# Optimization experiments

Measured on AMD Instinct MI355X. Metric: run time of the kernel, lower is better.

## Reference

```python
import jax, jax.numpy as jnp
import numpy as np

N_NODES = 50000
N_EDGES = 800000
IN_DIM = 64
HID = 64
N_CLASSES = 10
NUM_GRAPHS = 512
EPS = 1e-5


def setup_inputs() -> dict:
    key = jax.random.key(0)
    ks = jax.random.split(key, 24)
    def w(k, shape, fan_in):
        return jax.random.normal(k, shape, jnp.float32) / np.sqrt(fan_in)
    inp = {
        "input_feature": jax.random.normal(ks[0], (N_NODES, IN_DIM), jnp.float32),
        "edge_src": jax.random.randint(ks[1], (N_EDGES,), 0, N_NODES, jnp.int32),
        "edge_dst": jax.random.randint(ks[2], (N_EDGES,), 0, N_NODES, jnp.int32),
        "graph_indicator": jnp.sort(jax.random.randint(ks[3], (N_NODES,), 0, NUM_GRAPHS, jnp.int32)),
        "labels": jax.random.randint(ks[4], (NUM_GRAPHS,), 0, N_CLASSES, jnp.int32),
        # GraphSAGE layer weights (self + neighbor paths) and biases
        "Ws1": w(ks[5], (IN_DIM, HID), IN_DIM), "Wn1": w(ks[6], (IN_DIM, HID), IN_DIM), "b1": jnp.zeros((HID,), jnp.float32),
        "Ws2": w(ks[7], (HID, HID), HID), "Wn2": w(ks[8], (HID, HID), HID), "b2": jnp.zeros((HID,), jnp.float32),
        "Ws3": w(ks[9], (HID, HID), HID), "Wn3": w(ks[10], (HID, HID), HID), "b3": jnp.zeros((HID,), jnp.float32),
        # BatchNorm affine params (bn1 output is discarded by the original forward, so omitted)
        "g2": jnp.ones((HID,), jnp.float32), "be2": jnp.zeros((HID,), jnp.float32),
        "g3": jnp.ones((HID,), jnp.float32), "be3": jnp.zeros((HID,), jnp.float32),
        # MLP head
        "fcW1": w(ks[11], (HID, 2 * HID), HID), "fcb1": jnp.zeros((2 * HID,), jnp.float32),
        "fcW2": w(ks[12], (2 * HID, HID), 2 * HID), "fcb2": jnp.zeros((HID,), jnp.float32),
        "fcW3": w(ks[13], (HID, N_CLASSES), HID), "fcb3": jnp.zeros((N_CLASSES,), jnp.float32),
    }
    return inp


def _batchnorm(x, g, b):
    # training-mode BN over the node dimension
    m = jnp.mean(x, axis=0)
    v = jnp.var(x, axis=0)
    return (x - m) * jax.lax.rsqrt(v + EPS) * g + b


def _sage(x, Ws, Wn, b, src, dst, inv_deg):
    # mean-aggregate neighbor features: agg[i] = mean_{(j->i) in E} x[j]
    msg = x[src]                                                   # [E, d] gather
    agg = jax.ops.segment_sum(msg, dst, num_segments=N_NODES)       # [N, d] scatter-add
    agg = agg * inv_deg                                             # mean aggregation
    return jax.nn.relu(x @ Ws + agg @ Wn + b)


def reference(input_feature, edge_src, edge_dst, graph_indicator, labels,
              Ws1, Wn1, b1, Ws2, Wn2, b2, Ws3, Wn3, b3,
              g2, be2, g3, be3, fcW1, fcb1, fcW2, fcb2, fcW3, fcb3):
    deg = jax.ops.segment_sum(jnp.ones((N_EDGES,), jnp.float32), edge_dst, num_segments=N_NODES)
    inv_deg = (1.0 / jnp.maximum(deg, 1.0))[:, None]                # [N, 1]
    # NOTE: original forward computes bn1(input_feature) but discards it (dead code)
    h = _sage(input_feature, Ws1, Wn1, b1, edge_src, edge_dst, inv_deg)
    h = _batchnorm(h, g2, be2)
    h = _sage(h, Ws2, Wn2, b2, edge_src, edge_dst, inv_deg)
    h = _batchnorm(h, g3, be3)
    h = _sage(h, Ws3, Wn3, b3, edge_src, edge_dst, inv_deg)
    # sum-pool per graph (labels only determine the number of graphs)
    pooled = jax.ops.segment_sum(h, graph_indicator, num_segments=NUM_GRAPHS)  # [G, HID]
    h = jax.nn.relu(pooled @ fcW1 + fcb1)
    h = jax.nn.relu(h @ fcW2 + fcb2)
    logits = h @ fcW3 + fcb3                                        # [G, num_classes]
    return logits
```

## Files before the change

### kernel.cpp

```cpp
#include <hip/hip_runtime.h>

#define N_NODES   50000
#define N_EDGES   800000
#define DIM       64
#define NUM_GRAPHS 512
#define EPS       1e-5f

#define SB   1024
#define NSB  ((N_NODES + SB - 1) / SB)

#define NBUCK ((N_NODES + 255) >> 8)
#define PA_E  4096
#define PA_B  ((N_EDGES + PA_E - 1) / PA_E)

__global__ void k_zero(int* __restrict__ deg, float* __restrict__ sums2,
                       float* __restrict__ sums3, float* __restrict__ pooled) {
    int i = blockIdx.x * 256 + threadIdx.x;
    if (i < N_NODES) deg[i] = 0;
    if (i < 128) { sums2[i] = 0.f; sums3[i] = 0.f; }
    if (i < NUM_GRAPHS * DIM) pooled[i] = 0.f;
}

__global__ void k_count(const int* __restrict__ dst, int* __restrict__ deg) {
    int i = blockIdx.x * 256 + threadIdx.x;
    if (i < N_EDGES) atomicAdd(&deg[dst[i]], 1);
}

__global__ void __launch_bounds__(1024)
k_scan1(const int* __restrict__ deg, int* __restrict__ bsum) {
    __shared__ int red[16];
    int t = threadIdx.x;
    int i = blockIdx.x * SB + t;
    int v = (i < N_NODES) ? deg[i] : 0;
#pragma unroll
    for (int d = 32; d; d >>= 1) v += __shfl_down(v, d, 64);
    if ((t & 63) == 0) red[t >> 6] = v;
    __syncthreads();
    if (t < 16) {
        int s = red[t];
#pragma unroll
        for (int d = 8; d; d >>= 1) s += __shfl_down(s, d, 16);
        if (t == 0) bsum[blockIdx.x] = s;
    }
}

__global__ void k_scan2(const int* __restrict__ bsum, int* __restrict__ boff) {
    int t = threadIdx.x;
    int v = (t < NSB) ? bsum[t] : 0;
    int orig = v;
#pragma unroll
    for (int d = 1; d < 64; d <<= 1) {
        int u = __shfl_up(v, d, 64);
        if (t >= d) v += u;
    }
    if (t < NSB) boff[t] = v - orig;
}

__global__ void __launch_bounds__(1024)
k_scan3(const int* __restrict__ deg, const int* __restrict__ boff,
        int* __restrict__ off, float* __restrict__ invd) {
    __shared__ int wsum[16];
    int t = threadIdx.x, lane = t & 63, w = t >> 6;
    int i = blockIdx.x * SB + t;
    int d = (i < N_NODES) ? deg[i] : 0;
    int v = d;
#pragma unroll
    for (int s = 1; s < 64; s <<= 1) {
        int u = __shfl_up(v, s, 64);
        if (lane >= s) v += u;
    }
    if (lane == 63) wsum[w] = v;
    __syncthreads();
    if (t < 16) {
        int x = wsum[t];
#pragma unroll
        for (int s = 1; s < 16; s <<= 1) {
            int u = __shfl_up(x, s, 16);
            if (t >= s) x += u;
        }
        wsum[t] = x;
    }
    __syncthreads();
    if (i < N_NODES) {
        int ex = boff[blockIdx.x] + ((w > 0) ? wsum[w - 1] : 0) + v - d;
        off[i] = ex;
        invd[i] = 1.0f / (float)max(d, 1);
        if (i == N_NODES - 1) off[N_NODES] = ex + d;
    }
}

__global__ void k_bcinit(const int* __restrict__ off, int* __restrict__ bcur) {
    int t = blockIdx.x * 256 + threadIdx.x;
    if (t < NBUCK) bcur[t] = off[t << 8];
}

__global__ void __launch_bounds__(1024)
k_passA(const int* __restrict__ src, const int* __restrict__ dst,
        int* __restrict__ bcur, unsigned long long* __restrict__ ebuf) {
    __shared__ int hist[NBUCK];
    __shared__ int gbase[NBUCK];
    int t = threadIdx.x;
    for (int i = t; i < NBUCK; i += 1024) hist[i] = 0;
    __syncthreads();
    int e0 = blockIdx.x * PA_E;
    int s0, s1, s2, s3, d0, d1, d2, d3, l0, l1, l2, l3;
    bool v0, v1, v2, v3;
    {
        int e = e0 + t;
        v0 = e < N_EDGES;
        s0 = v0 ? src[min(e, N_EDGES - 1)] : 0;
        d0 = v0 ? dst[min(e, N_EDGES - 1)] : 0;
        l0 = v0 ? atomicAdd(&hist[d0 >> 8], 1) : 0;
    }
    {
        int e = e0 + t + 1024;
        v1 = e < N_EDGES;
        s1 = v1 ? src[min(e, N_EDGES - 1)] : 0;
        d1 = v1 ? dst[min(e, N_EDGES - 1)] : 0;
        l1 = v1 ? atomicAdd(&hist[d1 >> 8], 1) : 0;
    }
    {
        int e = e0 + t + 2048;
        v2 = e < N_EDGES;
        s2 = v2 ? src[min(e, N_EDGES - 1)] : 0;
        d2 = v2 ? dst[min(e, N_EDGES - 1)] : 0;
        l2 = v2 ? atomicAdd(&hist[d2 >> 8], 1) : 0;
    }
    {
        int e = e0 + t + 3072;
        v3 = e < N_EDGES;
        s3 = v3 ? src[min(e, N_EDGES - 1)] : 0;
        d3 = v3 ? dst[min(e, N_EDGES - 1)] : 0;
        l3 = v3 ? atomicAdd(&hist[d3 >> 8], 1) : 0;
    }
    __syncthreads();
    if (t < NBUCK) {
        int h = hist[t];
        gbase[t] = h ? atomicAdd(&bcur[t], h) : 0;
    }
    __syncthreads();
    if (v0) ebuf[gbase[d0 >> 8] + l0] = ((unsigned long long)d0 << 32) | (unsigned)s0;
    if (v1) ebuf[gbase[d1 >> 8] + l1] = ((unsigned long long)d1 << 32) | (unsigned)s1;
    if (v2) ebuf[gbase[d2 >> 8] + l2] = ((unsigned long long)d2 << 32) | (unsigned)s2;
    if (v3) ebuf[gbase[d3 >> 8] + l3] = ((unsigned long long)d3 << 32) | (unsigned)s3;
}

__global__ void __launch_bounds__(1024)
k_passB(const unsigned long long* __restrict__ ebuf, const int* __restrict__ off,
        int* __restrict__ csr_src) {
    __shared__ int lcur[256];
    int base = blockIdx.x << 8;
    int nn = min(256, N_NODES - base);
    int t = threadIdx.x;
    if (t < nn) lcur[t] = off[base + t];
    __syncthreads();
    int js = off[base];
    int je = off[base + nn];
    for (int j = js + t; j < je; j += 1024) {
        unsigned long long pk = ebuf[j];
        int d = (int)(pk >> 32);
        int s = (int)(unsigned)pk;
        int pos = atomicAdd(&lcur[d - base], 1);
        csr_src[pos] = s;
    }
}

__device__ inline unsigned short f2bf(float f) {
    unsigned u = __float_as_uint(f);
    return (unsigned short)((u + 0x7FFFu + ((u >> 16) & 1u)) >> 16);
}

#define GR 32
template<bool BN>
__global__ void __launch_bounds__(256)
k_gemm(const float* __restrict__ x, const float* __restrict__ Ws,
       const float* __restrict__ Wn, const float* __restrict__ bias,
       const float* __restrict__ bn_a, const float* __restrict__ bn_c,
       float* __restrict__ xs, unsigned short* __restrict__ xnh16) {
    __shared__ float sX[GR][DIM];
    int tid = threadIdx.x;
    int lane = tid & 63, w = tid >> 6;

    float wsr[DIM], wnr[DIM];
#pragma unroll
    for (int k = 0; k < DIM; ++k) {
        wsr[k] = Ws[k * DIM + lane];
        wnr[k] = Wn[k * DIM + lane];
    }
    float bv = bias[lane];
    float aL = 1.f, cL = 0.f;
    if constexpr (BN) { aL = bn_a[lane]; cL = bn_c[lane]; }

    int rowBase = blockIdx.x * GR;
#pragma unroll
    for (int r = 0; r < GR / 4; ++r) {
        int row = r * 4 + w;
        int gr = rowBase + row;
        float v = (gr < N_NODES) ? x[gr * DIM + lane] : 0.f;
        sX[row][lane] = fmaf(v, aL, cL);
    }
    __syncthreads();

#pragma unroll
    for (int r = 0; r < 8; ++r) {
        int row = w * 8 + r;
        float s = bv, n = 0.f;
#pragma unroll
        for (int kg = 0; kg < DIM / 4; ++kg) {
            float4 xv = *reinterpret_cast<const float4*>(&sX[row][kg * 4]);
            s = fmaf(xv.x, wsr[kg * 4 + 0], s); n = fmaf(xv.x, wnr[kg * 4 + 0], n);
            s = fmaf(xv.y, wsr[kg * 4 + 1], s); n = fmaf(xv.y, wnr[kg * 4 + 1], n);
            s = fmaf(xv.z, wsr[kg * 4 + 2], s); n = fmaf(xv.z, wnr[kg * 4 + 2], n);
            s = fmaf(xv.w, wsr[kg * 4 + 3], s); n = fmaf(xv.w, wnr[kg * 4 + 3], n);
        }
        int grow = rowBase + row;
        if (grow < N_NODES) {
            xs[grow * DIM + lane] = s;
            xnh16[grow * DIM + lane] = f2bf(n);
        }
    }
}

template<bool POOL>
__global__ void __launch_bounds__(256)
k_agg(const float* __restrict__ xs, const unsigned* __restrict__ xnh,
      const int* __restrict__ off, const int* __restrict__ csr_src,
      const float* __restrict__ inv_deg, const int* __restrict__ gind,
      float* __restrict__ h, float* __restrict__ pooled) {
    int tid = threadIdx.x;
    int w = tid >> 6;
    int lane = tid & 63;
    int hw = lane >> 5;
    int p = lane & 31;
    int half_id = blockIdx.x * 8 + w * 2 + hw;
    int rA = half_id * 2;
    int rB = rA + 1;
    int jA = off[rA], jeA = off[rA + 1];
    int jB = jeA,     jeB = off[rB + 1];
    float axA = 0.f, ayA = 0.f, axB = 0.f, ayB = 0.f;

    while (jA < jeA || jB < jeB) {
#pragma unroll
        for (int k = 0; k < 4; ++k) {
            int iA = jA + k, iB = jB + k;
            bool vA = iA < jeA, vB = iB < jeB;
            int sA = csr_src[min(iA, N_EDGES - 1)];
            int sB = csr_src[min(iB, N_EDGES - 1)];
            sA = vA ? sA : 0;
            sB = vB ? sB : 0;
            unsigned wA = xnh[sA * 32 + p];
            unsigned wB = xnh[sB * 32 + p];
            axA += vA ? __uint_as_float(wA << 16) : 0.f;
            ayA += vA ? __uint_as_float(wA & 0xFFFF0000u) : 0.f;
            axB += vB ? __uint_as_float(wB << 16) : 0.f;
            ayB += vB ? __uint_as_float(wB & 0xFFFF0000u) : 0.f;
        }
        jA += 4; jB += 4;
    }

    float idA = inv_deg[rA], idB = inv_deg[rB];
    float2 xvA = *reinterpret_cast<const float2*>(&xs[rA * DIM + 2 * p]);
    float2 xvB = *reinterpret_cast<const float2*>(&xs[rB * DIM + 2 * p]);
    float vxA = fmaxf(fmaf(axA, idA, xvA.x), 0.f);
    float vyA = fmaxf(fmaf(ayA, idA, xvA.y), 0.f);
    float vxB = fmaxf(fmaf(axB, idB, xvB.x), 0.f);
    float vyB = fmaxf(fmaf(ayB, idB, xvB.y), 0.f);
    *reinterpret_cast<float2*>(&h[rA * DIM + 2 * p]) = make_float2(vxA, vyA);
    *reinterpret_cast<float2*>(&h[rB * DIM + 2 * p]) = make_float2(vxB, vyB);
    if constexpr (POOL) {
        int gA = gind[rA], gB = gind[rB];
        atomicAdd(&pooled[gA * DIM + 2 * p], vxA);
        atomicAdd(&pooled[gA * DIM + 2 * p + 1], vyA);
        atomicAdd(&pooled[gB * DIM + 2 * p], vxB);
        atomicAdd(&pooled[gB * DIM + 2 * p + 1], vyB);
    }
}

__global__ void __launch_bounds__(256)
k_stats(const float* __restrict__ h, float* __restrict__ sums) {
    int lane = threadIdx.x & 63, w = threadIdx.x >> 6;
    float s = 0.f, q = 0.f;
    for (int r = blockIdx.x * 4 + w; r < N_NODES; r += gridDim.x * 4) {
        float v = h[r * DIM + lane];
        s += v;
        q = fmaf(v, v, q);
    }
    __shared__ float sS[4][DIM], sQ[4][DIM];
    sS[w][lane] = s; sQ[w][lane] = q;
    __syncthreads();
    if (w == 0) {
        float ts = sS[0][lane] + sS[1][lane] + sS[2][lane] + sS[3][lane];
        float tq = sQ[0][lane] + sQ[1][lane] + sQ[2][lane] + sQ[3][lane];
        atomicAdd(&sums[lane], ts);
        atomicAdd(&sums[DIM + lane], tq);
    }
}

__global__ void k_bnfin(const float* __restrict__ sums, const float* __restrict__ g,
                        const float* __restrict__ be, float* __restrict__ a,
                        float* __restrict__ c) {
    int t = threadIdx.x;
    float m = sums[t] * (1.0f / N_NODES);
    float q = sums[DIM + t] * (1.0f / N_NODES);
    float v = q - m * m;
    float inv = 1.0f / sqrtf(v + EPS);
    float av = g[t] * inv;
    a[t] = av;
    c[t] = be[t] - m * av;
}

__global__ void __launch_bounds__(128)
k_mlp(const float* __restrict__ pooled,
      const float* __restrict__ W1, const float* __restrict__ b1,
      const float* __restrict__ W2, const float* __restrict__ b2,
      const float* __restrict__ W3, const float* __restrict__ b3,
      float* __restrict__ out) {
    __shared__ float sp[64], s1[128], s2[64];
    int g = blockIdx.x, t = threadIdx.x;
    if (t < 64) sp[t] = pooled[g * 64 + t];
    __syncthreads();
    {
        float acc = b1[t];
#pragma unroll
        for (int k = 0; k < 64; ++k) acc = fmaf(sp[k], W1[k * 128 + t], acc);
        s1[t] = fmaxf(acc, 0.f);
    }
    __syncthreads();
    if (t < 64) {
        float acc = b2[t];
#pragma unroll
        for (int k = 0; k < 128; ++k) acc = fmaf(s1[k], W2[k * 64 + t], acc);
        s2[t] = fmaxf(acc, 0.f);
    }
    __syncthreads();
    if (t < 10) {
        float acc = b3[t];
#pragma unroll
        for (int k = 0; k < 64; ++k) acc = fmaf(s2[k], W3[k * 10 + t], acc);
        out[g * 10 + t] = acc;
    }
}

extern "C" void kernel_launch(void* const* d_in, const int* in_sizes, int n_in,
                              void* d_out, int out_size, void* d_ws, size_t ws_size,
                              hipStream_t stream) {
    const float* x0   = (const float*)d_in[0];
    const int* e_src  = (const int*)d_in[1];
    const int* e_dst  = (const int*)d_in[2];
    const int* gind   = (const int*)d_in[3];
    const float* Ws1 = (const float*)d_in[5],  *Wn1 = (const float*)d_in[6],  *b1 = (const float*)d_in[7];
    const float* Ws2 = (const float*)d_in[8],  *Wn2 = (const float*)d_in[9],  *b2 = (const float*)d_in[10];
    const float* Ws3 = (const float*)d_in[11], *Wn3 = (const float*)d_in[12], *b3 = (const float*)d_in[13];
    const float* g2  = (const float*)d_in[14], *be2 = (const float*)d_in[15];
    const float* g3  = (const float*)d_in[16], *be3 = (const float*)d_in[17];
    const float* fcW1 = (const float*)d_in[18], *fcb1 = (const float*)d_in[19];
    const float* fcW2 = (const float*)d_in[20], *fcb2 = (const float*)d_in[21];
    const float* fcW3 = (const float*)d_in[22], *fcb3 = (const float*)d_in[23];
    float* out = (float*)d_out;

    char* p = (char*)d_ws;
    auto carve = [&](size_t bytes) { void* r = (void*)p; p += (bytes + 255) & ~(size_t)255; return r; };
    int*   deg     = (int*)  carve(N_NODES * 4);
    int*   off     = (int*)  carve((N_NODES + 1) * 4);
    int*   csr_src = (int*)  carve(N_EDGES * 4);
    float* invd    = (float*)carve(N_NODES * 4);
    int*   bsum    = (int*)  carve(NSB * 4);
    int*   boff    = (int*)  carve((NSB + 1) * 4);
    int*   bcur    = (int*)  carve(NBUCK * 4);
    float* sums2   = (float*)carve(128 * 4);
    float* sums3   = (float*)carve(128 * 4);
    float* a2      = (float*)carve(64 * 4);
    float* c2      = (float*)carve(64 * 4);
    float* a3      = (float*)carve(64 * 4);
    float* c3      = (float*)carve(64 * 4);
    float* pooled  = (float*)carve(NUM_GRAPHS * DIM * 4);
    float* bufH    = (float*)carve((size_t)N_NODES * DIM * 4);
    float* bufXS   = (float*)carve((size_t)N_NODES * DIM * 4);
    unsigned* bufXN = (unsigned*)carve((size_t)N_NODES * 32 * 4);
    unsigned long long* ebuf = (unsigned long long*)carve((size_t)N_EDGES * 8);

    const int EB = (N_EDGES + 255) / 256;
    const int GB = (N_NODES + GR - 1) / GR;
    const int AB2 = N_NODES / 16;

    k_zero<<<(N_NODES + 255) / 256, 256, 0, stream>>>(deg, sums2, sums3, pooled);
    k_count<<<EB, 256, 0, stream>>>(e_dst, deg);
    k_scan1<<<NSB, SB, 0, stream>>>(deg, bsum);
    k_scan2<<<1, 64, 0, stream>>>(bsum, boff);
    k_scan3<<<NSB, SB, 0, stream>>>(deg, boff, off, invd);
    k_bcinit<<<1, 256, 0, stream>>>(off, bcur);
    k_passA<<<PA_B, 1024, 0, stream>>>(e_src, e_dst, bcur, ebuf);
    k_passB<<<NBUCK, 1024, 0, stream>>>(ebuf, off, csr_src);

    k_gemm<false><<<GB, 256, 0, stream>>>(x0, Ws1, Wn1, b1, nullptr, nullptr,
                                          bufXS, (unsigned short*)bufXN);
    k_agg<false><<<AB2, 256, 0, stream>>>(bufXS, bufXN, off, csr_src, invd, nullptr, bufH, nullptr);

    k_stats<<<240, 256, 0, stream>>>(bufH, sums2);
    k_bnfin<<<1, 64, 0, stream>>>(sums2, g2, be2, a2, c2);
    k_gemm<true><<<GB, 256, 0, stream>>>(bufH, Ws2, Wn2, b2, a2, c2,
                                         bufXS, (unsigned short*)bufXN);
    k_agg<false><<<AB2, 256, 0, stream>>>(bufXS, bufXN, off, csr_src, invd, nullptr, bufH, nullptr);

    k_stats<<<240, 256, 0, stream>>>(bufH, sums3);
    k_bnfin<<<1, 64, 0, stream>>>(sums3, g3, be3, a3, c3);
    k_gemm<true><<<GB, 256, 0, stream>>>(bufH, Ws3, Wn3, b3, a3, c3,
                                         bufXS, (unsigned short*)bufXN);
    k_agg<true><<<AB2, 256, 0, stream>>>(bufXS, bufXN, off, csr_src, invd, gind, bufH, pooled);

    k_mlp<<<NUM_GRAPHS, 128, 0, stream>>>(pooled, fcW1, fcb1, fcW2, fcb2, fcW3, fcb3, out);
}
```

Before: 300.9 us.

## Split bf16 neighbor table into two column slices and aggregate per slice

The GEMM now writes the bf16 neighbor projections as two separate 32-column tables, each 3.2 MB, instead of one interleaved 64-column table. Aggregation runs as two launches, one per slice, so each pass's random-gather working set is half as large and more likely to stay cache-resident. Each row is handled by 32 lanes that split its edges by parity and combine partial sums with a shuffle. The cost is twice the edge-index reads, twice the launches, and 32-byte gathers per edge instead of 64-byte.

```diff
diff --git a/kernel.cpp b/kernel.cpp
--- a/kernel.cpp
+++ b/kernel.cpp
@@ -191,6 +191,8 @@
     float aL = 1.f, cL = 0.f;
     if constexpr (BN) { aL = bn_a[lane]; cL = bn_c[lane]; }
 
+    unsigned short* nbase = xnh16 + (lane >> 5) * (N_NODES * 32) + (lane & 31);
+
     int rowBase = blockIdx.x * GR;
 #pragma unroll
     for (int r = 0; r < GR / 4; ++r) {
@@ -216,63 +218,56 @@
         int grow = rowBase + row;
         if (grow < N_NODES) {
             xs[grow * DIM + lane] = s;
-            xnh16[grow * DIM + lane] = f2bf(n);
+            nbase[grow * 32] = f2bf(n);
         }
     }
 }
 
-template<bool POOL>
+template<bool POOL, int SLICE>
 __global__ void __launch_bounds__(256)
-k_agg(const float* __restrict__ xs, const unsigned* __restrict__ xnh,
-      const int* __restrict__ off, const int* __restrict__ csr_src,
-      const float* __restrict__ inv_deg, const int* __restrict__ gind,
-      float* __restrict__ h, float* __restrict__ pooled) {
+k_agg2(const float* __restrict__ xs, const unsigned* __restrict__ tbl,
+       const int* __restrict__ off, const int* __restrict__ csr_src,
+       const float* __restrict__ inv_deg, const int* __restrict__ gind,
+       float* __restrict__ h, float* __restrict__ pooled) {
     int tid = threadIdx.x;
     int w = tid >> 6;
     int lane = tid & 63;
-    int hw = lane >> 5;
-    int p = lane & 31;
-    int half_id = blockIdx.x * 8 + w * 2 + hw;
-    int rA = half_id * 2;
+    int e = lane >> 4;
+    int p = lane & 15;
+    int rA = (blockIdx.x * 4 + w) * 2;
     int rB = rA + 1;
-    int jA = off[rA], jeA = off[rA + 1];
-    int jB = jeA,     jeB = off[rB + 1];
-    float axA = 0.f, ayA = 0.f, axB = 0.f, ayB = 0.f;
-
-    while (jA < jeA || jB < jeB) {
+    int row = (e < 2) ? rA : rB;
+    int par = e & 1;
+    int j = off[row] + par;
+    int je = off[row + 1];
+    float ax = 0.f, ay = 0.f;
+    while (j < je) {
 #pragma unroll
         for (int k = 0; k < 4; ++k) {
-            int iA = jA + k, iB = jB + k;
-            bool vA = iA < jeA, vB = iB < jeB;
-            int sA = csr_src[min(iA, N_EDGES - 1)];
-            int sB = csr_src[min(iB, N_EDGES - 1)];
-            sA = vA ? sA : 0;
-            sB = vB ? sB : 0;
-            unsigned wA = xnh[sA * 32 + p];
-            unsigned wB = xnh[sB * 32 + p];
-            axA += vA ? __uint_as_float(wA << 16) : 0.f;
-            ayA += vA ? __uint_as_float(wA & 0xFFFF0000u) : 0.f;
-            axB += vB ? __uint_as_float(wB << 16) : 0.f;
-            ayB += vB ? __uint_as_float(wB & 0xFFFF0000u) : 0.f;
+            int i = j + 2 * k;
+            bool v = i < je;
+            int s = csr_src[min(i, N_EDGES - 1)];
+            s = v ? s : 0;
+            unsigned wd = tbl[s * 16 + p];
+            ax += v ? __uint_as_float(wd << 16) : 0.f;
+            ay += v ? __uint_as_float(wd & 0xFFFF0000u) : 0.f;
         }
-        jA += 4; jB += 4;
-    }
-
-    float idA = inv_deg[rA], idB = inv_deg[rB];
-    float2 xvA = *reinterpret_cast<const float2*>(&xs[rA * DIM + 2 * p]);
-    float2 xvB = *reinterpret_cast<const float2*>(&xs[rB * DIM + 2 * p]);
-    float vxA = fmaxf(fmaf(axA, idA, xvA.x), 0.f);
-    float vyA = fmaxf(fmaf(ayA, idA, xvA.y), 0.f);
-    float vxB = fmaxf(fmaf(axB, idB, xvB.x), 0.f);
-    float vyB = fmaxf(fmaf(ayB, idB, xvB.y), 0.f);
-    *reinterpret_cast<float2*>(&h[rA * DIM + 2 * p]) = make_float2(vxA, vyA);
-    *reinterpret_cast<float2*>(&h[rB * DIM + 2 * p]) = make_float2(vxB, vyB);
-    if constexpr (POOL) {
-        int gA = gind[rA], gB = gind[rB];
-        atomicAdd(&pooled[gA * DIM + 2 * p], vxA);
-        atomicAdd(&pooled[gA * DIM + 2 * p + 1], vyA);
-        atomicAdd(&pooled[gB * DIM + 2 * p], vxB);
-        atomicAdd(&pooled[gB * DIM + 2 * p + 1], vyB);
+        j += 8;
+    }
+    ax += __shfl_xor(ax, 16, 64);
+    ay += __shfl_xor(ay, 16, 64);
+    if (par == 0) {
+        float id = inv_deg[row];
+        int cbase = row * DIM + SLICE * 32 + 2 * p;
+        float2 xv = *reinterpret_cast<const float2*>(&xs[cbase]);
+        float vx = fmaxf(fmaf(ax, id, xv.x), 0.f);
+        float vy = fmaxf(fmaf(ay, id, xv.y), 0.f);
+        *reinterpret_cast<float2*>(&h[cbase]) = make_float2(vx, vy);
+        if constexpr (POOL) {
+            int g = gind[row];
+            atomicAdd(&pooled[g * DIM + SLICE * 32 + 2 * p], vx);
+            atomicAdd(&pooled[g * DIM + SLICE * 32 + 2 * p + 1], vy);
+        }
     }
 }
 
@@ -379,9 +374,12 @@
     unsigned* bufXN = (unsigned*)carve((size_t)N_NODES * 32 * 4);
     unsigned long long* ebuf = (unsigned long long*)carve((size_t)N_EDGES * 8);
 
+    const unsigned* tbl0 = bufXN;
+    const unsigned* tbl1 = bufXN + (size_t)N_NODES * 16;
+
     const int EB = (N_EDGES + 255) / 256;
     const int GB = (N_NODES + GR - 1) / GR;
-    const int AB2 = N_NODES / 16;
+    const int AGB = (N_NODES + 7) / 8;
 
     k_zero<<<(N_NODES + 255) / 256, 256, 0, stream>>>(deg, sums2, sums3, pooled);
     k_count<<<EB, 256, 0, stream>>>(e_dst, deg);
@@ -394,19 +392,22 @@
 
     k_gemm<false><<<GB, 256, 0, stream>>>(x0, Ws1, Wn1, b1, nullptr, nullptr,
                                           bufXS, (unsigned short*)bufXN);
-    k_agg<false><<<AB2, 256, 0, stream>>>(bufXS, bufXN, off, csr_src, invd, nullptr, bufH, nullptr);
+    k_agg2<false, 0><<<AGB, 256, 0, stream>>>(bufXS, tbl0, off, csr_src, invd, nullptr, bufH, nullptr);
+    k_agg2<false, 1><<<AGB, 256, 0, stream>>>(bufXS, tbl1, off, csr_src, invd, nullptr, bufH, nullptr);
 
     k_stats<<<240, 256, 0, stream>>>(bufH, sums2);
     k_bnfin<<<1, 64, 0, stream>>>(sums2, g2, be2, a2, c2);
     k_gemm<true><<<GB, 256, 0, stream>>>(bufH, Ws2, Wn2, b2, a2, c2,
                                          bufXS, (unsigned short*)bufXN);
-    k_agg<false><<<AB2, 256, 0, stream>>>(bufXS, bufXN, off, csr_src, invd, nullptr, bufH, nullptr);
+    k_agg2<false, 0><<<AGB, 256, 0, stream>>>(bufXS, tbl0, off, csr_src, invd, nullptr, bufH, nullptr);
+    k_agg2<false, 1><<<AGB, 256, 0, stream>>>(bufXS, tbl1, off, csr_src, invd, nullptr, bufH, nullptr);
 
     k_stats<<<240, 256, 0, stream>>>(bufH, sums3);
     k_bnfin<<<1, 64, 0, stream>>>(sums3, g3, be3, a3, c3);
     k_gemm<true><<<GB, 256, 0, stream>>>(bufH, Ws3, Wn3, b3, a3, c3,
                                          bufXS, (unsigned short*)bufXN);
-    k_agg<true><<<AB2, 256, 0, stream>>>(bufXS, bufXN, off, csr_src, invd, gind, bufH, pooled);
+    k_agg2<true, 0><<<AGB, 256, 0, stream>>>(bufXS, tbl0, off, csr_src, invd, gind, bufH, pooled);
+    k_agg2<true, 1><<<AGB, 256, 0, stream>>>(bufXS, tbl1, off, csr_src, invd, gind, bufH, pooled);
 
     k_mlp<<<NUM_GRAPHS, 128, 0, stream>>>(pooled, fcW1, fcb1, fcW2, fcb2, fcW3, fcb3, out);
 }
```

Result: slower. 323.8 us (+7.6%).
